# Optimization experiments

Hardware: AMD Instinct MI355X
Metric: run time of the kernel (lower is better)

## Reference

```python
import jax, jax.numpy as jnp
import numpy as np

B, Q, KV, D, H = 2, 2048, 2048, 1024, 16
HD = D // H  # head dim = 64


def setup_inputs() -> dict:
    key = jax.random.key(0)
    ks = jax.random.split(key, 16)
    s = 1.0 / np.sqrt(D)
    return {
        "q": jax.random.normal(ks[0], (B, Q, D), jnp.float32),
        "k": jax.random.normal(ks[1], (B, KV, D), jnp.float32),
        "v": jax.random.normal(ks[2], (B, KV, D), jnp.float32),
        "past_k": jax.random.normal(ks[3], (B, KV, D), jnp.float32),
        "past_v": jax.random.normal(ks[4], (B, KV, D), jnp.float32),
        "mask": jax.random.randint(ks[5], (B, Q, KV + KV), 0, 2).astype(bool),
        "Wq": jax.random.uniform(ks[6], (D, D), jnp.float32, -s, s),
        "bq": jax.random.uniform(ks[7], (D,), jnp.float32, -s, s),
        "Wk": jax.random.uniform(ks[8], (D, D), jnp.float32, -s, s),
        "bk": jax.random.uniform(ks[9], (D,), jnp.float32, -s, s),
        "Wv": jax.random.uniform(ks[10], (D, D), jnp.float32, -s, s),
        "bv": jax.random.uniform(ks[11], (D,), jnp.float32, -s, s),
        "Wl": jax.random.uniform(ks[12], (D, D), jnp.float32, -s, s),
        "bl": jax.random.uniform(ks[13], (D,), jnp.float32, -s, s),
    }


def _split_heads(x):
    # (B, S, D) -> (B, H, S, HD)
    b, s, _ = x.shape
    return x.reshape(b, s, H, HD).transpose(0, 2, 1, 3)


def reference(q, k, v, past_k, past_v, mask, Wq, bq, Wk, bk, Wv, bv, Wl, bl):
    qp = q @ Wq.T + bq
    kp = k @ Wk.T + bk
    vp = v @ Wv.T + bv
    k_cat = jnp.concatenate([past_k, kp], axis=-2)  # (B, P+KV, D)
    v_cat = jnp.concatenate([past_v, vp], axis=-2)
    qh = _split_heads(qp)        # (B, H, Q, HD)
    kh = _split_heads(k_cat)     # (B, H, P+KV, HD)
    vh = _split_heads(v_cat)
    scores = jnp.einsum("bhqd,bhkd->bhqk", qh, kh) / np.sqrt(HD)
    scores = scores + mask[:, None].astype(scores.dtype) * (-10000.0)
    attn = jax.nn.softmax(scores, axis=-1)
    out = jnp.einsum("bhqk,bhkd->bhqd", attn, vh)  # (B, H, Q, HD)
    out = out.transpose(0, 2, 1, 3).reshape(q.shape[0], q.shape[1], D)
    x = out @ Wl.T + bl
    return (x, k_cat, v_cat)
```

## Files before the change

kernel.cpp:

```cpp
#include <hip/hip_runtime.h>

#define QLEN 2048
#define KVTOT 4096
#define DMODEL 1024
#define MASKC2 -14427.0f
#define SENT2  -28854.0f

typedef __attribute__((ext_vector_type(8))) short bf16x8;
typedef __attribute__((ext_vector_type(4))) float f32x4;
typedef unsigned short u16;
typedef unsigned int u32;
typedef unsigned long long u64;

__device__ __forceinline__ u16 f2b(float f) {
  union { float f; unsigned u; } v; v.f = f;
  unsigned r = v.u + 0x7FFFu + ((v.u >> 16) & 1u);
  return (u16)(r >> 16);
}

__device__ __forceinline__ float b2f(u16 x) {
  union { u32 u; float f; } v; v.u = (u32)x << 16; return v.f;
}

__device__ __forceinline__ u32 cvt_pk_bf16(float lo, float hi) {
  u32 r;
  asm("v_cvt_pk_bf16_f32 %0, %1, %2" : "=v"(r) : "v"(lo), "v"(hi));
  return r;
}

__device__ __forceinline__ float exp2v(float x) {
  float r;
  asm("v_exp_f32 %0, %1" : "=v"(r) : "v"(x));
  return r;
}

__device__ __forceinline__ float max3f(float a, float b, float c) {
  float r;
  asm("v_max3_f32 %0, %1, %2, %3" : "=v"(r) : "v"(a), "v"(b), "v"(c));
  return r;
}

__device__ __forceinline__ void gll16(const u16* g, u16* l) {
  __builtin_amdgcn_global_load_lds(
      (const __attribute__((address_space(1))) u32*)g,
      (__attribute__((address_space(3))) u32*)l, 16, 0, 0);
}

__global__ __launch_bounds__(256) void copy_past(
    const float* __restrict__ pk, const float* __restrict__ pv,
    float* __restrict__ kcat, float* __restrict__ vcat,
    u16* __restrict__ kh) {
  int i = blockIdx.x * 256 + threadIdx.x;
  int b = i >> 19;
  int r = i & 524287;
  size_t src = (size_t)i * 4;
  size_t dst = ((size_t)b * 1048576 + r) * 4;
  float4 kk = *(const float4*)&pk[src];
  float4 vv = *(const float4*)&pv[src];
  *(float4*)&kcat[dst] = kk;
  *(float4*)&vcat[dst] = vv;
  int s = r >> 8;
  int c4 = (r & 255) * 4;
  int h = c4 >> 6, d = c4 & 63;
  uint2 w = make_uint2(cvt_pk_bf16(kk.x, kk.y), cvt_pk_bf16(kk.z, kk.w));
  *(uint2*)&kh[((size_t)(b * 16 + h) * KVTOT + s) * 64 + d] = w;
}

__global__ __launch_bounds__(256) void maskpack(
    const int* __restrict__ mask, u64* __restrict__ bits) {
  int w = blockIdx.x * 4 + (threadIdx.x >> 6);
  int lane = threadIdx.x & 63;
  int mv = mask[(size_t)w * 64 + lane];
  u64 b = __ballot(mv != 0);
  if (lane == 0) bits[w] = b;
}

__global__ __launch_bounds__(256) void w2b(
    const float* __restrict__ w0, const float* __restrict__ w1,
    const float* __restrict__ w2, const float* __restrict__ w3,
    u16* __restrict__ dst) {
  const float* src = blockIdx.y == 0 ? w0 : blockIdx.y == 1 ? w1
                   : blockIdx.y == 2 ? w2 : w3;
  size_t i = ((size_t)blockIdx.x * 256 + threadIdx.x) * 8;
  float4 a = *(const float4*)&src[i];
  float4 b = *(const float4*)&src[i + 4];
  uint4 o = {cvt_pk_bf16(a.x, a.y), cvt_pk_bf16(a.z, a.w),
             cvt_pk_bf16(b.x, b.y), cvt_pk_bf16(b.z, b.w)};
  *(uint4*)&dst[(size_t)blockIdx.y * 1048576 + i] = o;
}

__global__ __launch_bounds__(256) void a2b(
    const float* __restrict__ a0, const float* __restrict__ a1,
    const float* __restrict__ a2, u16* __restrict__ dst0,
    u16* __restrict__ dst12) {
  const int y = blockIdx.y;
  const float* src = y == 0 ? a0 : y == 1 ? a1 : a2;
  u16* dst = y == 0 ? dst0 : dst12 + (size_t)(y - 1) * 4194304;
  size_t i = ((size_t)blockIdx.x * 256 + threadIdx.x) * 8;
  float4 a = *(const float4*)&src[i];
  float4 b = *(const float4*)&src[i + 4];
  uint4 o = {cvt_pk_bf16(a.x, a.y), cvt_pk_bf16(a.z, a.w),
             cvt_pk_bf16(b.x, b.y), cvt_pk_bf16(b.z, b.w)};
  *(uint4*)&dst[i] = o;
}

__global__ __launch_bounds__(256) void gemm_qkv(
    const u16* __restrict__ Ab0, const u16* __restrict__ Ab12,
    const u16* __restrict__ Wb,
    const float* __restrict__ bq, const float* __restrict__ bk,
    const float* __restrict__ bv,
    u16* __restrict__ qh, float* __restrict__ kcat, u16* __restrict__ kh,
    float* __restrict__ vcat) {
  const int K = 1024, N = 1024;
  __shared__ u16 As[128][32];
  __shared__ u16 Bs[128][32];
  const int z = blockIdx.z;
  const u16* A = (z == 0) ? Ab0 : Ab12 + (size_t)(z - 1) * 4194304;
  const u16* W = Wb + (size_t)z * 1048576;
  const float* bias = (z == 0) ? bq : (z == 1) ? bk : bv;
  const int t = threadIdx.x;
  const int m0 = blockIdx.y * 128, n0 = blockIdx.x * 128;
  const int lane = t & 63, wid = t >> 6;
  const int wr = (wid >> 1) * 64, wc = (wid & 1) * 64;
  const int lr = lane & 15, lg = lane >> 4;
  const int ko = lg * 8;

  f32x4 acc[4][4];
  #pragma unroll
  for (int m = 0; m < 4; ++m)
    #pragma unroll
    for (int n = 0; n < 4; ++n)
      acc[m][n] = (f32x4){0.f, 0.f, 0.f, 0.f};

  for (int k0 = 0; k0 < K; k0 += 32) {
    __syncthreads();
    #pragma unroll
    for (int j = 0; j < 2; ++j) {
      int idx = t + j * 256;
      int r = idx >> 2, c8 = (idx & 3) * 8;
      size_t ldsoff = (size_t)(j * 256 + (t & ~63)) * 8;
      gll16(A + (size_t)(m0 + r) * K + k0 + c8, &As[0][0] + ldsoff);
      gll16(W + (size_t)(n0 + r) * K + k0 + c8, &Bs[0][0] + ldsoff);
    }
    __syncthreads();
    bf16x8 av[4], bv4[4];
    #pragma unroll
    for (int m = 0; m < 4; ++m)
      av[m] = *(const bf16x8*)&As[wr + m * 16 + lr][ko];
    #pragma unroll
    for (int n = 0; n < 4; ++n)
      bv4[n] = *(const bf16x8*)&Bs[wc + n * 16 + lr][ko];
    #pragma unroll
    for (int m = 0; m < 4; ++m)
      #pragma unroll
      for (int n = 0; n < 4; ++n)
        acc[m][n] = __builtin_amdgcn_mfma_f32_16x16x32_bf16(av[m], bv4[n], acc[m][n], 0, 0, 0);
  }

  const int rq = lg * 4;
  #pragma unroll
  for (int m = 0; m < 4; ++m) {
    #pragma unroll
    for (int r = 0; r < 4; ++r) {
      int row = m0 + wr + m * 16 + rq + r;
      int bb = row >> 11, s = row & 2047;
      #pragma unroll
      for (int n = 0; n < 4; ++n) {
        int col = n0 + wc + n * 16 + lr;
        float val = acc[m][n][r] + bias[col];
        int hh = col >> 6, d = col & 63;
        if (z == 0) {
          qh[((size_t)(bb * 16 + hh) * QLEN + s) * 64 + d] = f2b(val * 0.18033688f);
        } else if (z == 1) {
          kcat[(size_t)(bb * 4096 + 2048 + s) * 1024 + col] = val;
          kh[((size_t)(bb * 16 + hh) * KVTOT + 2048 + s) * 64 + d] = f2b(val);
        } else {
          vcat[(size_t)(bb * 4096 + 2048 + s) * 1024 + col] = val;
        }
      }
    }
  }
}

__global__ __launch_bounds__(256) void gemm_out(
    const u16* __restrict__ A, const u16* __restrict__ W,
    const float* __restrict__ bias, float* __restrict__ C) {
  const int K = 1024, N = 1024;
  __shared__ u16 As[128][32];
  __shared__ u16 Bs[128][32];
  const int t = threadIdx.x;
  const int m0 = blockIdx.y * 128, n0 = blockIdx.x * 128;
  const int lane = t & 63, wid = t >> 6;
  const int wr = (wid >> 1) * 64, wc = (wid & 1) * 64;
  const int lr = lane & 15, lg = lane >> 4;
  const int ko = lg * 8;

  f32x4 acc[4][4];
  #pragma unroll
  for (int m = 0; m < 4; ++m)
    #pragma unroll
    for (int n = 0; n < 4; ++n)
      acc[m][n] = (f32x4){0.f, 0.f, 0.f, 0.f};

  for (int k0 = 0; k0 < K; k0 += 32) {
    __syncthreads();
    #pragma unroll
    for (int j = 0; j < 2; ++j) {
      int idx = t + j * 256;
      int r = idx >> 2, c8 = (idx & 3) * 8;
      size_t ldsoff = (size_t)(j * 256 + (t & ~63)) * 8;
      gll16(A + (size_t)(m0 + r) * K + k0 + c8, &As[0][0] + ldsoff);
      gll16(W + (size_t)(n0 + r) * K + k0 + c8, &Bs[0][0] + ldsoff);
    }
    __syncthreads();
    bf16x8 av[4], bv4[4];
    #pragma unroll
    for (int m = 0; m < 4; ++m)
      av[m] = *(const bf16x8*)&As[wr + m * 16 + lr][ko];
    #pragma unroll
    for (int n = 0; n < 4; ++n)
      bv4[n] = *(const bf16x8*)&Bs[wc + n * 16 + lr][ko];
    #pragma unroll
    for (int m = 0; m < 4; ++m)
      #pragma unroll
      for (int n = 0; n < 4; ++n)
        acc[m][n] = __builtin_amdgcn_mfma_f32_16x16x32_bf16(av[m], bv4[n], acc[m][n], 0, 0, 0);
  }

  const int rq = lg * 4;
  #pragma unroll
  for (int m = 0; m < 4; ++m) {
    #pragma unroll
    for (int r = 0; r < 4; ++r) {
      int row = m0 + wr + m * 16 + rq + r;
      float* cp = C + (size_t)row * N;
      #pragma unroll
      for (int n = 0; n < 4; ++n) {
        int col = n0 + wc + n * 16 + lr;
        cp[col] = acc[m][n][r] + bias[col];
      }
    }
  }
}

__global__ __launch_bounds__(256) void repack_vt(
    const float* __restrict__ src, u16* __restrict__ dst) {
  __shared__ u16 T[64][72];
  const int t = threadIdx.x;
  const int kv0 = blockIdx.x * 64;
  const int bh = blockIdx.y;
  const int b = bh >> 4, h = bh & 15;
  #pragma unroll
  for (int it = 0; it < 4; ++it) {
    int idx = t + it * 256;
    int r = idx >> 4;
    int c4 = (idx & 15) * 4;
    float4 v = *(const float4*)(src + (size_t)(b * KVTOT + kv0 + r) * DMODEL + h * 64 + c4);
    *(uint2*)&T[r][c4] = make_uint2(cvt_pk_bf16(v.x, v.y), cvt_pk_bf16(v.z, v.w));
  }
  __syncthreads();
  #pragma unroll
  for (int it = 0; it < 2; ++it) {
    int idx = t + it * 256;
    int d = idx & 63;
    int kc8 = (idx >> 6) * 8;
    bf16x8 o;
    #pragma unroll
    for (int j = 0; j < 8; ++j) o[j] = (short)T[kc8 + j][d];
    *(bf16x8*)(dst + (size_t)((b * 16 + h) * 64 + d) * KVTOT + kv0 + kc8) = o;
  }
}

__global__ __launch_bounds__(256, 2) void attn_mfma(
    const u16* __restrict__ qh, const u16* __restrict__ kh,
    const u16* __restrict__ vt, const u64* __restrict__ mbits,
    u16* __restrict__ out) {
  __shared__ __align__(16) u16 shm[4 * 64 * 72];
  __shared__ float mM[4][64];
  __shared__ float mL[4][64];
  const int t = threadIdx.x;
  const int wid = t >> 6, lane = t & 63;
  const int lr = lane & 15, lg = lane >> 4;
  const int fid = blockIdx.x;
  const int virt = (fid & 7) * 128 + (fid >> 3);
  const int bh = virt >> 5, qt = virt & 31;
  const int b = bh >> 4, h = bh & 15;
  const int q0 = qt * 64;

  u16* bufA = shm + wid * 2304;
  u16* bufB = bufA + 1152;

  bf16x8 ones;
  #pragma unroll
  for (int j = 0; j < 8; ++j) ones[j] = (short)0x3F80;

  bf16x8 qf[4][2];
  #pragma unroll
  for (int i = 0; i < 4; ++i) {
    const u16* qp = qh + ((size_t)bh * QLEN + q0 + i * 16 + lr) * 64 + lg * 8;
    qf[i][0] = *(const bf16x8*)qp;
    qf[i][1] = *(const bf16x8*)(qp + 32);
  }

  const u16* kbase = kh + (size_t)bh * KVTOT * 64 + (size_t)wid * 1024 * 64;
  const u16* vbase = vt + (size_t)bh * 64 * KVTOT + wid * 1024;
  const u64* mbase = mbits + ((size_t)b * QLEN + q0 + lr) * 64 + wid * 16;

  float mprev[4] = {SENT2, SENT2, SENT2, SENT2};
  f32x4 oacc[4][4];
  f32x4 oaccL[4];
  #pragma unroll
  for (int i = 0; i < 4; ++i) {
    oaccL[i] = (f32x4){0.f, 0.f, 0.f, 0.f};
    #pragma unroll
    for (int dt = 0; dt < 4; ++dt) oacc[i][dt] = (f32x4){0.f, 0.f, 0.f, 0.f};
  }

  bf16x8 kf[4][2];
  #pragma unroll
  for (int tile = 0; tile < 4; ++tile) {
    const u16* kp = kbase + (size_t)(tile * 16 + lr) * 64 + lg * 8;
    kf[tile][0] = *(const bf16x8*)kp;
    kf[tile][1] = *(const bf16x8*)(kp + 32);
  }

  bf16x8 vf[4][2];

  auto QK = [&](int i, f32x4* sacc, u64 mb) {
    u64 mq = mb >> (lg * 4);
    const float negm = -mprev[i], negmm = MASKC2 - mprev[i];
    #pragma unroll
    for (int tile = 0; tile < 4; ++tile) {
      unsigned nib = (unsigned)((mq >> (tile * 16)) & 0xFull);
      #pragma unroll
      for (int r = 0; r < 4; ++r)
        sacc[tile][r] = (nib & (1u << r)) ? negmm : negm;
    }
    __builtin_amdgcn_s_setprio(1);
    #pragma unroll
    for (int tile = 0; tile < 4; ++tile) {
      sacc[tile] = __builtin_amdgcn_mfma_f32_16x16x32_bf16(kf[tile][0], qf[i][0], sacc[tile], 0, 0, 0);
      sacc[tile] = __builtin_amdgcn_mfma_f32_16x16x32_bf16(kf[tile][1], qf[i][1], sacc[tile], 0, 0, 0);
    }
    __builtin_amdgcn_s_setprio(0);
  };

  auto SM = [&](int i, f32x4* sacc, u16* pbuf) {
    float t1 = max3f(sacc[0][0], sacc[0][1], sacc[0][2]);
    float t2 = max3f(sacc[0][3], sacc[1][0], sacc[1][1]);
    float t3 = max3f(sacc[1][2], sacc[1][3], sacc[2][0]);
    float t4 = max3f(sacc[2][1], sacc[2][2], sacc[2][3]);
    float t5 = max3f(sacc[3][0], sacc[3][1], sacc[3][2]);
    float lmax = fmaxf(sacc[3][3], t1);
    lmax = max3f(lmax, t2, t3);
    lmax = max3f(lmax, t4, t5);
    if (!__all(lmax <= 11.0f)) {
      float rmax = fmaxf(lmax, __shfl_xor(lmax, 16));
      rmax = fmaxf(rmax, __shfl_xor(rmax, 32));
      float shift = fmaxf(rmax, 0.f);
      float corr = exp2v(-shift);
      float cr[4];
      #pragma unroll
      for (int r = 0; r < 4; ++r) cr[r] = __shfl(corr, lg * 4 + r);
      #pragma unroll
      for (int dt = 0; dt < 4; ++dt)
        #pragma unroll
        for (int r = 0; r < 4; ++r) oacc[i][dt][r] *= cr[r];
      #pragma unroll
      for (int r = 0; r < 4; ++r) oaccL[i][r] *= cr[r];
      mprev[i] += shift;
      #pragma unroll
      for (int tile = 0; tile < 4; ++tile)
        #pragma unroll
        for (int r = 0; r < 4; ++r) sacc[tile][r] -= shift;
    }
    #pragma unroll
    for (int tile = 0; tile < 4; ++tile) {
      float p0 = exp2v(sacc[tile][0]);
      float p1 = exp2v(sacc[tile][1]);
      float p2 = exp2v(sacc[tile][2]);
      float p3 = exp2v(sacc[tile][3]);
      *(uint2*)&pbuf[lr * 72 + tile * 16 + lg * 4] =
          make_uint2(cvt_pk_bf16(p0, p1), cvt_pk_bf16(p2, p3));
    }
  };

  auto PV = [&](int i, const u16* pbuf) {
    bf16x8 pa0 = *(const bf16x8*)&pbuf[lr * 72 + lg * 8];
    bf16x8 pa1 = *(const bf16x8*)&pbuf[lr * 72 + 32 + lg * 8];
    __builtin_amdgcn_s_setprio(1);
    #pragma unroll
    for (int dt = 0; dt < 4; ++dt) {
      oacc[i][dt] = __builtin_amdgcn_mfma_f32_16x16x32_bf16(pa0, vf[dt][0], oacc[i][dt], 0, 0, 0);
      oacc[i][dt] = __builtin_amdgcn_mfma_f32_16x16x32_bf16(pa1, vf[dt][1], oacc[i][dt], 0, 0, 0);
    }
    oaccL[i] = __builtin_amdgcn_mfma_f32_16x16x32_bf16(pa0, ones, oaccL[i], 0, 0, 0);
    oaccL[i] = __builtin_amdgcn_mfma_f32_16x16x32_bf16(pa1, ones, oaccL[i], 0, 0, 0);
    __builtin_amdgcn_s_setprio(0);
  };

  f32x4 sA[4], sB[4];

  for (int it = 0; it < 16; ++it) {
    u64 mbv[4];
    #pragma unroll
    for (int i = 0; i < 4; ++i) mbv[i] = mbase[(size_t)i * 1024 + it];

    const u16* vp = vbase + it * 64;
    #pragma unroll
    for (int dt = 0; dt < 4; ++dt) {
      const u16* vq = vp + (size_t)(dt * 16 + lr) * KVTOT + lg * 8;
      vf[dt][0] = *(const bf16x8*)vq;
      vf[dt][1] = *(const bf16x8*)(vq + 32);
    }

    QK(0, sA, mbv[0]);
    SM(0, sA, bufA);
    QK(1, sB, mbv[1]);
    PV(0, bufA);
    SM(1, sB, bufB);
    QK(2, sA, mbv[2]);
    PV(1, bufB);
    SM(2, sA, bufA);
    QK(3, sB, mbv[3]);
    if (it + 1 < 16) {
      const u16* kp = kbase + (size_t)(it + 1) * 4096;
      #pragma unroll
      for (int tile = 0; tile < 4; ++tile) {
        const u16* kq = kp + (size_t)(tile * 16 + lr) * 64 + lg * 8;
        kf[tile][0] = *(const bf16x8*)kq;
        kf[tile][1] = *(const bf16x8*)(kq + 32);
      }
    }
    PV(2, bufA);
    SM(3, sB, bufB);
    PV(3, bufB);
  }

  __syncthreads();
  u16* mo = shm + wid * 4608;
  #pragma unroll
  for (int i = 0; i < 4; ++i)
    #pragma unroll
    for (int dt = 0; dt < 4; ++dt)
      #pragma unroll
      for (int r = 0; r < 4; ++r)
        mo[(i * 16 + lg * 4 + r) * 72 + dt * 16 + lr] = f2b(oacc[i][dt][r]);
  if (lr == 0) {
    #pragma unroll
    for (int i = 0; i < 4; ++i)
      #pragma unroll
      for (int r = 0; r < 4; ++r)
        mL[wid][i * 16 + lg * 4 + r] = oaccL[i][r];
  }
  if (lg == 0) {
    #pragma unroll
    for (int i = 0; i < 4; ++i) mM[wid][i * 16 + lr] = mprev[i];
  }
  __syncthreads();

  const int q = wid * 16 + lr;
  float m0 = mM[0][q], m1 = mM[1][q], m2 = mM[2][q], m3 = mM[3][q];
  float mm = fmaxf(max3f(m0, m1, m2), m3);
  float w0 = exp2v(m0 - mm), w1 = exp2v(m1 - mm);
  float w2 = exp2v(m2 - mm), w3 = exp2v(m3 - mm);
  float l = mL[0][q] * w0 + mL[1][q] * w1 + mL[2][q] * w2 + mL[3][q] * w3;
  float inv = 1.f / l;
  float wgt[4] = {w0 * inv, w1 * inv, w2 * inv, w3 * inv};
  float o[16];
  #pragma unroll
  for (int j = 0; j < 16; ++j) o[j] = 0.f;
  #pragma unroll
  for (int w = 0; w < 4; ++w) {
    const u16* src = shm + w * 4608 + q * 72 + lg * 16;
    bf16x8 a0 = *(const bf16x8*)src;
    bf16x8 a1 = *(const bf16x8*)(src + 8);
    #pragma unroll
    for (int j = 0; j < 8; ++j) {
      o[j]     += b2f((u16)a0[j]) * wgt[w];
      o[8 + j] += b2f((u16)a1[j]) * wgt[w];
    }
  }
  u16* op = out + ((size_t)b * QLEN + q0 + q) * DMODEL + h * 64 + lg * 16;
  uint4 wA = {cvt_pk_bf16(o[0], o[1]), cvt_pk_bf16(o[2], o[3]),
              cvt_pk_bf16(o[4], o[5]), cvt_pk_bf16(o[6], o[7])};
  uint4 wB = {cvt_pk_bf16(o[8], o[9]), cvt_pk_bf16(o[10], o[11]),
              cvt_pk_bf16(o[12], o[13]), cvt_pk_bf16(o[14], o[15])};
  *(uint4*)op = wA;
  *(uint4*)(op + 8) = wB;
}

extern "C" void kernel_launch(void* const* d_in, const int* in_sizes, int n_in,
                              void* d_out, int out_size, void* d_ws, size_t ws_size,
                              hipStream_t stream) {
  const float* q      = (const float*)d_in[0];
  const float* k      = (const float*)d_in[1];
  const float* v      = (const float*)d_in[2];
  const float* past_k = (const float*)d_in[3];
  const float* past_v = (const float*)d_in[4];
  const int*   mask   = (const int*)d_in[5];
  const float* Wq     = (const float*)d_in[6];
  const float* bq     = (const float*)d_in[7];
  const float* Wk     = (const float*)d_in[8];
  const float* bk     = (const float*)d_in[9];
  const float* Wv     = (const float*)d_in[10];
  const float* bv     = (const float*)d_in[11];
  const float* Wl     = (const float*)d_in[12];
  const float* bl     = (const float*)d_in[13];

  float* xout = (float*)d_out;
  float* kcat = xout + 4194304;
  float* vcat = xout + 12582912;

  u16* wsb = (u16*)d_ws;
  u16* attno = wsb;
  u16* qh = wsb + 4194304;
  u16* kh = wsb + 8388608;
  u16* vt = wsb + 16777216;
  u16* Wb = wsb + 25165824;
  u64* mbits = (u64*)(wsb + 29360128);

  copy_past<<<4096, 256, 0, stream>>>(past_k, past_v, kcat, vcat, kh);
  maskpack<<<65536, 256, 0, stream>>>(mask, mbits);
  w2b<<<dim3(512, 4), 256, 0, stream>>>(Wq, Wk, Wv, Wl, Wb);
  a2b<<<dim3(2048, 3), 256, 0, stream>>>(q, k, v, attno, vt);

  gemm_qkv<<<dim3(8, 32, 3), 256, 0, stream>>>(
      attno, vt, Wb, bq, bk, bv, qh, kcat, kh, vcat);

  repack_vt<<<dim3(64, 32), 256, 0, stream>>>(vcat, vt);

  attn_mfma<<<1024, 256, 0, stream>>>(qh, kh, vt, mbits, attno);

  gemm_out<<<dim3(8, 32), 256, 0, stream>>>(attno, Wb + 3145728, bl, xout);
}
```

Measured before the change: 301.4 us.

## Restructure attention to per-wave query rows with shared LDS-staged K/V tiles

Reorganizes the attention kernel so each wave owns 16 query rows over the full KV range, replacing the previous split where each wave handled a quarter of KV for all 64 queries and merged partial softmax results at the end. K and V tiles are loaded once per block into double-buffered, XOR-swizzled LDS with async global-to-LDS copies (gll16), and all four waves read them from there. This drops the cross-wave merge of max and sum and the duplicated direct global loads per wave. The cost is a block barrier every iteration, more LDS traffic for fragment reads, and removal of the occupancy hint in the launch bounds.

Measured after the change: 324.5 us. 1.08x slower.

```diff
diff --git a/kernel.cpp b/kernel.cpp
--- a/kernel.cpp
+++ b/kernel.cpp
@@ -271,13 +271,12 @@
   }
 }
 
-__global__ __launch_bounds__(256, 2) void attn_mfma(
+__global__ __launch_bounds__(256) void attn_mfma(
     const u16* __restrict__ qh, const u16* __restrict__ kh,
     const u16* __restrict__ vt, const u64* __restrict__ mbits,
     u16* __restrict__ out) {
-  __shared__ __align__(16) u16 shm[4 * 64 * 72];
-  __shared__ float mM[4][64];
-  __shared__ float mL[4][64];
+  __shared__ __align__(16) u16 KV[2][2][64 * 64];
+  __shared__ __align__(16) u16 P[4][16 * 72];
   const int t = threadIdx.x;
   const int wid = t >> 6, lane = t & 63;
   const int lr = lane & 15, lg = lane >> 4;
@@ -286,49 +285,60 @@
   const int bh = virt >> 5, qt = virt & 31;
   const int b = bh >> 4, h = bh & 15;
   const int q0 = qt * 64;
-
-  u16* bufA = shm + wid * 2304;
-  u16* bufB = bufA + 1152;
+  const int qw = q0 + wid * 16;
+
+  u16* Pw = &P[wid][0];
 
   bf16x8 ones;
   #pragma unroll
   for (int j = 0; j < 8; ++j) ones[j] = (short)0x3F80;
 
-  bf16x8 qf[4][2];
-  #pragma unroll
-  for (int i = 0; i < 4; ++i) {
-    const u16* qp = qh + ((size_t)bh * QLEN + q0 + i * 16 + lr) * 64 + lg * 8;
-    qf[i][0] = *(const bf16x8*)qp;
-    qf[i][1] = *(const bf16x8*)(qp + 32);
-  }
-
-  const u16* kbase = kh + (size_t)bh * KVTOT * 64 + (size_t)wid * 1024 * 64;
-  const u16* vbase = vt + (size_t)bh * 64 * KVTOT + wid * 1024;
-  const u64* mbase = mbits + ((size_t)b * QLEN + q0 + lr) * 64 + wid * 16;
-
-  float mprev[4] = {SENT2, SENT2, SENT2, SENT2};
-  f32x4 oacc[4][4];
-  f32x4 oaccL[4];
-  #pragma unroll
-  for (int i = 0; i < 4; ++i) {
-    oaccL[i] = (f32x4){0.f, 0.f, 0.f, 0.f};
-    #pragma unroll
-    for (int dt = 0; dt < 4; ++dt) oacc[i][dt] = (f32x4){0.f, 0.f, 0.f, 0.f};
-  }
-
-  bf16x8 kf[4][2];
-  #pragma unroll
-  for (int tile = 0; tile < 4; ++tile) {
-    const u16* kp = kbase + (size_t)(tile * 16 + lr) * 64 + lg * 8;
-    kf[tile][0] = *(const bf16x8*)kp;
-    kf[tile][1] = *(const bf16x8*)(kp + 32);
-  }
-
-  bf16x8 vf[4][2];
-
-  auto QK = [&](int i, f32x4* sacc, u64 mb) {
-    u64 mq = mb >> (lg * 4);
-    const float negm = -mprev[i], negmm = MASKC2 - mprev[i];
+  bf16x8 qf0, qf1;
+  {
+    const u16* qp = qh + ((size_t)bh * QLEN + qw + lr) * 64 + lg * 8;
+    qf0 = *(const bf16x8*)qp;
+    qf1 = *(const bf16x8*)(qp + 32);
+  }
+
+  const size_t khb = (size_t)bh * KVTOT * 64;
+  const size_t vtb = (size_t)bh * 64 * KVTOT;
+  const u64* mrow = mbits + ((size_t)b * QLEN + qw + lr) * 64;
+
+  auto STAGE = [&](int bi, int t0) {
+    #pragma unroll
+    for (int j = 0; j < 2; ++j) {
+      int idx = t + j * 256;
+      int r = idx >> 3, c = idx & 7;
+      gll16(kh + khb + (size_t)(t0 + r) * 64 + ((c ^ (r & 7)) * 8),
+            &KV[bi][0][0] + (size_t)((t & ~63) + j * 256) * 8);
+      gll16(vt + vtb + (size_t)r * KVTOT + t0 + ((c ^ (r & 7)) * 8),
+            &KV[bi][1][0] + (size_t)((t & ~63) + j * 256) * 8);
+    }
+  };
+  auto LDF = [&](const u16* base, int row, int ch) -> bf16x8 {
+    return *(const bf16x8*)(base + row * 64 + ((ch ^ (row & 7)) * 8));
+  };
+
+  float mprev = SENT2;
+  f32x4 oacc[4];
+  f32x4 oaccL = (f32x4){0.f, 0.f, 0.f, 0.f};
+  #pragma unroll
+  for (int dt = 0; dt < 4; ++dt) oacc[dt] = (f32x4){0.f, 0.f, 0.f, 0.f};
+
+  STAGE(0, 0);
+  u64 mcur = mrow[0];
+  __syncthreads();
+
+  int cur = 0;
+  for (int it = 0; it < 64; ++it) {
+    const u16* klc = &KV[cur][0][0];
+    const u16* vlc = &KV[cur][1][0];
+    if (it + 1 < 64) STAGE(cur ^ 1, (it + 1) * 64);
+    u64 mnext = (it + 1 < 64) ? mrow[it + 1] : 0;
+
+    u64 mq = mcur >> (lg * 4);
+    const float negm = -mprev, negmm = MASKC2 - mprev;
+    f32x4 sacc[4];
     #pragma unroll
     for (int tile = 0; tile < 4; ++tile) {
       unsigned nib = (unsigned)((mq >> (tile * 16)) & 0xFull);
@@ -339,155 +349,82 @@
     __builtin_amdgcn_s_setprio(1);
     #pragma unroll
     for (int tile = 0; tile < 4; ++tile) {
-      sacc[tile] = __builtin_amdgcn_mfma_f32_16x16x32_bf16(kf[tile][0], qf[i][0], sacc[tile], 0, 0, 0);
-      sacc[tile] = __builtin_amdgcn_mfma_f32_16x16x32_bf16(kf[tile][1], qf[i][1], sacc[tile], 0, 0, 0);
+      bf16x8 k0 = LDF(klc, tile * 16 + lr, lg);
+      bf16x8 k1 = LDF(klc, tile * 16 + lr, 4 + lg);
+      sacc[tile] = __builtin_amdgcn_mfma_f32_16x16x32_bf16(k0, qf0, sacc[tile], 0, 0, 0);
+      sacc[tile] = __builtin_amdgcn_mfma_f32_16x16x32_bf16(k1, qf1, sacc[tile], 0, 0, 0);
     }
     __builtin_amdgcn_s_setprio(0);
-  };
-
-  auto SM = [&](int i, f32x4* sacc, u16* pbuf) {
-    float t1 = max3f(sacc[0][0], sacc[0][1], sacc[0][2]);
-    float t2 = max3f(sacc[0][3], sacc[1][0], sacc[1][1]);
-    float t3 = max3f(sacc[1][2], sacc[1][3], sacc[2][0]);
-    float t4 = max3f(sacc[2][1], sacc[2][2], sacc[2][3]);
-    float t5 = max3f(sacc[3][0], sacc[3][1], sacc[3][2]);
-    float lmax = fmaxf(sacc[3][3], t1);
-    lmax = max3f(lmax, t2, t3);
-    lmax = max3f(lmax, t4, t5);
-    if (!__all(lmax <= 11.0f)) {
-      float rmax = fmaxf(lmax, __shfl_xor(lmax, 16));
-      rmax = fmaxf(rmax, __shfl_xor(rmax, 32));
-      float shift = fmaxf(rmax, 0.f);
-      float corr = exp2v(-shift);
-      float cr[4];
-      #pragma unroll
-      for (int r = 0; r < 4; ++r) cr[r] = __shfl(corr, lg * 4 + r);
-      #pragma unroll
-      for (int dt = 0; dt < 4; ++dt)
+
+    {
+      float t1 = max3f(sacc[0][0], sacc[0][1], sacc[0][2]);
+      float t2 = max3f(sacc[0][3], sacc[1][0], sacc[1][1]);
+      float t3 = max3f(sacc[1][2], sacc[1][3], sacc[2][0]);
+      float t4 = max3f(sacc[2][1], sacc[2][2], sacc[2][3]);
+      float t5 = max3f(sacc[3][0], sacc[3][1], sacc[3][2]);
+      float lmax = fmaxf(sacc[3][3], t1);
+      lmax = max3f(lmax, t2, t3);
+      lmax = max3f(lmax, t4, t5);
+      if (!__all(lmax <= 11.0f)) {
+        float rmax = fmaxf(lmax, __shfl_xor(lmax, 16));
+        rmax = fmaxf(rmax, __shfl_xor(rmax, 32));
+        float shift = fmaxf(rmax, 0.f);
+        float corr = exp2v(-shift);
+        float cr[4];
         #pragma unroll
-        for (int r = 0; r < 4; ++r) oacc[i][dt][r] *= cr[r];
-      #pragma unroll
-      for (int r = 0; r < 4; ++r) oaccL[i][r] *= cr[r];
-      mprev[i] += shift;
-      #pragma unroll
-      for (int tile = 0; tile < 4; ++tile)
+        for (int r = 0; r < 4; ++r) cr[r] = __shfl(corr, lg * 4 + r);
         #pragma unroll
-        for (int r = 0; r < 4; ++r) sacc[tile][r] -= shift;
-    }
-    #pragma unroll
-    for (int tile = 0; tile < 4; ++tile) {
-      float p0 = exp2v(sacc[tile][0]);
-      float p1 = exp2v(sacc[tile][1]);
-      float p2 = exp2v(sacc[tile][2]);
-      float p3 = exp2v(sacc[tile][3]);
-      *(uint2*)&pbuf[lr * 72 + tile * 16 + lg * 4] =
-          make_uint2(cvt_pk_bf16(p0, p1), cvt_pk_bf16(p2, p3));
-    }
-  };
-
-  auto PV = [&](int i, const u16* pbuf) {
-    bf16x8 pa0 = *(const bf16x8*)&pbuf[lr * 72 + lg * 8];
-    bf16x8 pa1 = *(const bf16x8*)&pbuf[lr * 72 + 32 + lg * 8];
-    __builtin_amdgcn_s_setprio(1);
-    #pragma unroll
-    for (int dt = 0; dt < 4; ++dt) {
-      oacc[i][dt] = __builtin_amdgcn_mfma_f32_16x16x32_bf16(pa0, vf[dt][0], oacc[i][dt], 0, 0, 0);
-      oacc[i][dt] = __builtin_amdgcn_mfma_f32_16x16x32_bf16(pa1, vf[dt][1], oacc[i][dt], 0, 0, 0);
-    }
-    oaccL[i] = __builtin_amdgcn_mfma_f32_16x16x32_bf16(pa0, ones, oaccL[i], 0, 0, 0);
-    oaccL[i] = __builtin_amdgcn_mfma_f32_16x16x32_bf16(pa1, ones, oaccL[i], 0, 0, 0);
-    __builtin_amdgcn_s_setprio(0);
-  };
-
-  f32x4 sA[4], sB[4];
-
-  for (int it = 0; it < 16; ++it) {
-    u64 mbv[4];
-    #pragma unroll
-    for (int i = 0; i < 4; ++i) mbv[i] = mbase[(size_t)i * 1024 + it];
-
-    const u16* vp = vbase + it * 64;
-    #pragma unroll
-    for (int dt = 0; dt < 4; ++dt) {
-      const u16* vq = vp + (size_t)(dt * 16 + lr) * KVTOT + lg * 8;
-      vf[dt][0] = *(const bf16x8*)vq;
-      vf[dt][1] = *(const bf16x8*)(vq + 32);
-    }
-
-    QK(0, sA, mbv[0]);
-    SM(0, sA, bufA);
-    QK(1, sB, mbv[1]);
-    PV(0, bufA);
-    SM(1, sB, bufB);
-    QK(2, sA, mbv[2]);
-    PV(1, bufB);
-    SM(2, sA, bufA);
-    QK(3, sB, mbv[3]);
-    if (it + 1 < 16) {
-      const u16* kp = kbase + (size_t)(it + 1) * 4096;
+        for (int dt = 0; dt < 4; ++dt)
+          #pragma unroll
+          for (int r = 0; r < 4; ++r) oacc[dt][r] *= cr[r];
+        #pragma unroll
+        for (int r = 0; r < 4; ++r) oaccL[r] *= cr[r];
+        mprev += shift;
+        #pragma unroll
+        for (int tile = 0; tile < 4; ++tile)
+          #pragma unroll
+          for (int r = 0; r < 4; ++r) sacc[tile][r] -= shift;
+      }
       #pragma unroll
       for (int tile = 0; tile < 4; ++tile) {
-        const u16* kq = kp + (size_t)(tile * 16 + lr) * 64 + lg * 8;
-        kf[tile][0] = *(const bf16x8*)kq;
-        kf[tile][1] = *(const bf16x8*)(kq + 32);
+        float p0 = exp2v(sacc[tile][0]);
+        float p1 = exp2v(sacc[tile][1]);
+        float p2 = exp2v(sacc[tile][2]);
+        float p3 = exp2v(sacc[tile][3]);
+        *(uint2*)&Pw[lr * 72 + tile * 16 + lg * 4] =
+            make_uint2(cvt_pk_bf16(p0, p1), cvt_pk_bf16(p2, p3));
       }
     }
-    PV(2, bufA);
-    SM(3, sB, bufB);
-    PV(3, bufB);
-  }
-
-  __syncthreads();
-  u16* mo = shm + wid * 4608;
-  #pragma unroll
-  for (int i = 0; i < 4; ++i)
+
+    {
+      bf16x8 pa0 = *(const bf16x8*)&Pw[lr * 72 + lg * 8];
+      bf16x8 pa1 = *(const bf16x8*)&Pw[lr * 72 + 32 + lg * 8];
+      __builtin_amdgcn_s_setprio(1);
+      #pragma unroll
+      for (int dt = 0; dt < 4; ++dt) {
+        bf16x8 v0 = LDF(vlc, dt * 16 + lr, lg);
+        bf16x8 v1 = LDF(vlc, dt * 16 + lr, 4 + lg);
+        oacc[dt] = __builtin_amdgcn_mfma_f32_16x16x32_bf16(pa0, v0, oacc[dt], 0, 0, 0);
+        oacc[dt] = __builtin_amdgcn_mfma_f32_16x16x32_bf16(pa1, v1, oacc[dt], 0, 0, 0);
+      }
+      oaccL = __builtin_amdgcn_mfma_f32_16x16x32_bf16(pa0, ones, oaccL, 0, 0, 0);
+      oaccL = __builtin_amdgcn_mfma_f32_16x16x32_bf16(pa1, ones, oaccL, 0, 0, 0);
+      __builtin_amdgcn_s_setprio(0);
+    }
+
+    mcur = mnext;
+    __syncthreads();
+    cur ^= 1;
+  }
+
+  #pragma unroll
+  for (int r = 0; r < 4; ++r) {
+    float inv = 1.f / oaccL[r];
+    u16* op = out + ((size_t)b * QLEN + qw + lg * 4 + r) * DMODEL + h * 64 + lr;
     #pragma unroll
     for (int dt = 0; dt < 4; ++dt)
-      #pragma unroll
-      for (int r = 0; r < 4; ++r)
-        mo[(i * 16 + lg * 4 + r) * 72 + dt * 16 + lr] = f2b(oacc[i][dt][r]);
-  if (lr == 0) {
-    #pragma unroll
-    for (int i = 0; i < 4; ++i)
-      #pragma unroll
-      for (int r = 0; r < 4; ++r)
-        mL[wid][i * 16 + lg * 4 + r] = oaccL[i][r];
-  }
-  if (lg == 0) {
-    #pragma unroll
-    for (int i = 0; i < 4; ++i) mM[wid][i * 16 + lr] = mprev[i];
-  }
-  __syncthreads();
-
-  const int q = wid * 16 + lr;
-  float m0 = mM[0][q], m1 = mM[1][q], m2 = mM[2][q], m3 = mM[3][q];
-  float mm = fmaxf(max3f(m0, m1, m2), m3);
-  float w0 = exp2v(m0 - mm), w1 = exp2v(m1 - mm);
-  float w2 = exp2v(m2 - mm), w3 = exp2v(m3 - mm);
-  float l = mL[0][q] * w0 + mL[1][q] * w1 + mL[2][q] * w2 + mL[3][q] * w3;
-  float inv = 1.f / l;
-  float wgt[4] = {w0 * inv, w1 * inv, w2 * inv, w3 * inv};
-  float o[16];
-  #pragma unroll
-  for (int j = 0; j < 16; ++j) o[j] = 0.f;
-  #pragma unroll
-  for (int w = 0; w < 4; ++w) {
-    const u16* src = shm + w * 4608 + q * 72 + lg * 16;
-    bf16x8 a0 = *(const bf16x8*)src;
-    bf16x8 a1 = *(const bf16x8*)(src + 8);
-    #pragma unroll
-    for (int j = 0; j < 8; ++j) {
-      o[j]     += b2f((u16)a0[j]) * wgt[w];
-      o[8 + j] += b2f((u16)a1[j]) * wgt[w];
-    }
-  }
-  u16* op = out + ((size_t)b * QLEN + q0 + q) * DMODEL + h * 64 + lg * 16;
-  uint4 wA = {cvt_pk_bf16(o[0], o[1]), cvt_pk_bf16(o[2], o[3]),
-              cvt_pk_bf16(o[4], o[5]), cvt_pk_bf16(o[6], o[7])};
-  uint4 wB = {cvt_pk_bf16(o[8], o[9]), cvt_pk_bf16(o[10], o[11]),
-              cvt_pk_bf16(o[12], o[13]), cvt_pk_bf16(o[14], o[15])};
-  *(uint4*)op = wA;
-  *(uint4*)(op + 8) = wB;
+      op[dt * 16] = f2b(oacc[dt][r] * inv);
+  }
 }
 
 extern "C" void kernel_launch(void* const* d_in, const int* in_sizes, int n_in,
```
